# Kernel tuning notes

Measured on AMD Instinct MI355X. Metric: run time of the kernel, lower is better.

Reference implementation:

```python
import jax, jax.numpy as jnp
import numpy as np

N_HEAD, D_MODEL, D_HEAD = 16, 1024, 64
SEQ, BATCH = 2048, 2
EPS = 1e-5


def layer_norm(x, g, b):
    mu = jnp.mean(x, axis=-1, keepdims=True)
    var = jnp.var(x, axis=-1, keepdims=True)
    return (x - mu) * jax.lax.rsqrt(var + EPS) * g + b


def pos_table(n_rows, d_model):
    pos = jnp.arange(n_rows, dtype=jnp.float32)[:, None]
    freqs = jnp.power(10000.0, -jnp.arange(0, d_model, 2, dtype=jnp.float32) / d_model)
    ang = pos * freqs  # [n_rows, d_model//2]
    tab = jnp.zeros((n_rows, d_model), dtype=jnp.float32)
    tab = tab.at[:, 0::2].set(jnp.sin(ang))
    tab = tab.at[:, 1::2].set(jnp.cos(ang))
    return tab


def setup_inputs() -> dict:
    key = jax.random.key(0)
    ks = jax.random.split(key, 7)
    s = 0.02
    return {
        "dec_inp": jax.random.normal(ks[0], (SEQ, BATCH, D_MODEL), jnp.float32),
        "Wq": jax.random.normal(ks[1], (N_HEAD * D_HEAD, D_MODEL), jnp.float32) * s,
        "Wkv": jax.random.normal(ks[2], (2 * N_HEAD * D_HEAD, D_MODEL), jnp.float32) * s,
        "Wo": jax.random.normal(ks[3], (D_MODEL, N_HEAD * D_HEAD), jnp.float32) * s,
        "g1": jnp.ones((D_MODEL,), jnp.float32),
        "b1": jnp.zeros((D_MODEL,), jnp.float32),
        "Wff": jax.random.normal(ks[4], (D_MODEL, N_HEAD * D_HEAD), jnp.float32) * s,
        "g2": jnp.ones((D_MODEL,), jnp.float32),
        "b2": jnp.zeros((D_MODEL,), jnp.float32),
    }


def reference(dec_inp, Wq, Wkv, Wo, g1, b1, Wff, g2, b2):
    S, B, D = dec_inp.shape
    scale = 1.0 / (D_HEAD ** 0.5)
    # projections (post-lnorm path, no mems: c == h)
    q = jnp.einsum('ibd,ed->ibe', dec_inp, Wq).reshape(S, B, N_HEAD, D_HEAD)
    kv = jnp.einsum('ibd,ed->ibe', dec_inp, Wkv)
    k, v = jnp.split(kv, 2, axis=-1)
    k = k.reshape(S, B, N_HEAD, D_HEAD)
    v = v.reshape(S, B, N_HEAD, D_HEAD)
    # attention: scores [i, j, b, n], softmax over j (dim=1)
    scores = jnp.einsum('ibnd,jbnd->ijbn', q, k) * scale
    prob = jax.nn.softmax(scores, axis=1)
    vec = jnp.einsum('ijbn,jbnd->ibnd', prob, v).reshape(S, B, N_HEAD * D_HEAD)
    attn_out = jnp.einsum('ibe,de->ibd', vec, Wo)
    out = layer_norm(dec_inp + attn_out, g1, b1)
    # output += ff(output)
    out = out + jnp.einsum('ibe,de->ibd', out, Wff)
    out = layer_norm(out, g2, b2)
    # output += pos_emb(output)  ==  2*out + pe  (pe indexed by shape[1]==batch)
    pe = pos_table(B, D)  # [B, D], broadcasts over seq
    return out + (out + pe)
```

## Files before the change

kernel.cpp:

```cpp
#include <hip/hip_runtime.h>
#include <hip/hip_bf16.h>
#include <math.h>


typedef __bf16 bf16x8 __attribute__((ext_vector_type(8)));
typedef float f32x4  __attribute__((ext_vector_type(4)));

typedef const __attribute__((address_space(1))) unsigned int as1_uint;
typedef __attribute__((address_space(3))) unsigned int as3_uint;

constexpr int S_SEQ = 2048;
constexpr int DH    = 64;

#define WS_MB (1ull << 20)

__device__ __forceinline__ void gload16(void* lds, const void* g) {
  __builtin_amdgcn_global_load_lds((as1_uint*)g, (as3_uint*)lds, 16, 0, 0);
}

__device__ __forceinline__ float fast_exp2(float x) {
  float r;
  asm volatile("v_exp_f32 %0, %1\n\ts_nop 1" : "=v"(r) : "v"(x));
  return r;
}
__device__ __forceinline__ unsigned cvt_pk_bf16(float lo, float hi) {
  unsigned r;
  asm("v_cvt_pk_bf16_f32 %0, %1, %2" : "=v"(r) : "v"(lo), "v"(hi));
  return r;
}

__device__ __forceinline__ void cvt4(const float* __restrict__ in,
                                     __hip_bfloat16* __restrict__ out, int idx) {
  float4 v = ((const float4*)in)[idx];
  uint2 p;
  p.x = cvt_pk_bf16(v.x, v.y);
  p.y = cvt_pk_bf16(v.z, v.w);
  *(uint2*)(out + (size_t)idx * 4) = p;
}

__global__ __launch_bounds__(256)
void prep_kernel(const float* __restrict__ x, const float* __restrict__ Wq,
                 const float* __restrict__ Wkv, const float* __restrict__ Wo,
                 const float* __restrict__ Wff,
                 __hip_bfloat16* __restrict__ Xb,
                 __hip_bfloat16* __restrict__ Wqkv_b,
                 __hip_bfloat16* __restrict__ Wo_b,
                 __hip_bfloat16* __restrict__ Wff_b,
                 float* __restrict__ pe) {
  const int bid = blockIdx.x, t = threadIdx.x;
  if (bid < 4096) {
    cvt4(x, Xb, bid * 256 + t);
  } else if (bid < 5120) {
    cvt4(Wq, Wqkv_b, (bid - 4096) * 256 + t);
  } else if (bid < 7168) {
    cvt4(Wkv, Wqkv_b + 1024 * 1024, (bid - 5120) * 256 + t);
  } else if (bid < 8192) {
    cvt4(Wo, Wo_b, (bid - 7168) * 256 + t);
  } else if (bid < 9216) {
    cvt4(Wff, Wff_b, (bid - 8192) * 256 + t);
  } else {
#pragma unroll
    for (int rep = 0; rep < 2; ++rep) {
      const int k = rep * 256 + t;
      float freq = expf(-(2.0f * (float)k / 1024.0f) * logf(10000.0f));
      pe[2 * k]            = 0.0f;
      pe[2 * k + 1]        = 1.0f;
      pe[1024 + 2 * k]     = sinf(freq);
      pe[1024 + 2 * k + 1] = cosf(freq);
    }
  }
}

template <int MODE, int BN>
__global__ __launch_bounds__(256)
void gemm_bt(const __hip_bfloat16* __restrict__ A,
             const __hip_bfloat16* __restrict__ Bw,
             float* __restrict__ C,
             __hip_bfloat16* __restrict__ Qb,
             __hip_bfloat16* __restrict__ Kb,
             __hip_bfloat16* __restrict__ VTb,
             int Ndim, int Kdim) {
  constexpr int ASZ = 128 * 64 * 2;
  constexpr int BSZ = BN * 64 * 2;
  constexpr int NI  = BN / 32;
  __shared__ __align__(16) char smem[2 * (ASZ + BSZ)];
  const int t = threadIdx.x, w = t >> 6, l = t & 63;
  const int bm = blockIdx.y * 128, bn = blockIdx.x * BN;
  const int m0 = (w >> 1) * 64, n0 = (w & 1) * (BN / 2);
  const int lrow = l >> 3, lcol = l & 7;
  const int ll = l & 15, lg = l >> 4;

  auto stage = [&](char* buf, int kt) {
#pragma unroll
    for (int r = 0; r < 4; ++r) {
      const int chunk = r * 4 + w;
      const int row = chunk * 8 + lrow;
      gload16(buf + chunk * 1024 + l * 16,
              A + (size_t)(bm + row) * Kdim + kt + lcol * 8);
    }
#pragma unroll
    for (int r = 0; r < BN / 32; ++r) {
      const int chunk = r * 4 + w;
      const int row = chunk * 8 + lrow;
      gload16(buf + ASZ + chunk * 1024 + l * 16,
              Bw + (size_t)(bn + row) * Kdim + kt + lcol * 8);
    }
  };

  f32x4 acc[4][NI] = {};

  stage(smem, 0);
  __syncthreads();
  int cur = 0;
  for (int kt = 0; kt < Kdim; kt += 64) {
    char* bufc = smem + cur * (ASZ + BSZ);
    if (kt + 64 < Kdim) stage(smem + (cur ^ 1) * (ASZ + BSZ), kt + 64);
    const char* sA = bufc;
    const char* sB = bufc + ASZ;
#pragma unroll
    for (int ks = 0; ks < 2; ++ks) {
      bf16x8 a[4], bfr[NI];
#pragma unroll
      for (int mi = 0; mi < 4; ++mi)
        a[mi] = *(const bf16x8*)(sA + (m0 + mi * 16 + ll) * 128 + ks * 64 + lg * 16);
#pragma unroll
      for (int ni = 0; ni < NI; ++ni)
        bfr[ni] = *(const bf16x8*)(sB + (n0 + ni * 16 + ll) * 128 + ks * 64 + lg * 16);
#pragma unroll
      for (int mi = 0; mi < 4; ++mi)
#pragma unroll
        for (int ni = 0; ni < NI; ++ni)
          acc[mi][ni] = __builtin_amdgcn_mfma_f32_16x16x32_bf16(
              a[mi], bfr[ni], acc[mi][ni], 0, 0, 0);
    }
    __syncthreads();
    cur ^= 1;
  }

  if (MODE == 0) {
#pragma unroll
    for (int mi = 0; mi < 4; ++mi)
#pragma unroll
      for (int ni = 0; ni < NI; ++ni)
#pragma unroll
        for (int r = 0; r < 4; ++r) {
          const int gm = bm + m0 + mi * 16 + lg * 4 + r;
          const int gn = bn + n0 + ni * 16 + ll;
          C[(size_t)gm * Ndim + gn] = acc[mi][ni][r];
        }
  } else {
    __hip_bfloat16* img = (__hip_bfloat16*)smem;
    const bool isV = (bn >= 2048);
#pragma unroll
    for (int mi = 0; mi < 4; ++mi)
#pragma unroll
      for (int ni = 0; ni < NI; ++ni)
#pragma unroll
        for (int r = 0; r < 4; ++r) {
          const int gml = m0 + mi * 16 + lg * 4 + r;
          const int gnl = n0 + ni * 16 + ll;
          const int off = isV ? gnl * 136 + ((gml & 1) << 6) + (gml >> 1)
                              : gml * 136 + gnl;
          img[off] = __float2bfloat16(acc[mi][ni][r]);
        }
    __syncthreads();
    const int i0 = bm >> 1;
    const int tile0 = bm >> 6;
#pragma unroll
    for (int j = 0; j < 8; ++j) {
      const int c = j * 256 + t;
      uint4 val;
      __hip_bfloat16* dst;
      if (bn < 1024) {
        const int bb = c >> 10, hl = (c >> 9) & 1;
        const int q = c & 511, il = q >> 3, dh0 = (q & 7) * 8;
        val = *(const uint4*)&img[(il * 2 + bb) * 136 + hl * 64 + dh0];
        dst = Qb + ((size_t)(bb * 16 + (bn >> 6) + hl) * 2048 + i0 + il) * 64 + dh0;
      } else if (bn < 2048) {
        const int run = c >> 6, lane = c & 63;
        const int bb = run >> 4, hl = (run >> 3) & 1, th = (run >> 2) & 1,
                  instr = run & 3;
        const int lg2 = lane >> 4, ll2 = lane & 15;
        const int r32 = (ll2 >> 2) * 8 + (ll2 & 3) + ((instr >> 1) << 2);
        const int il = th * 32 + r32;
        const int dh0 = (instr & 1) * 32 + lg2 * 8;
        val = *(const uint4*)&img[(il * 2 + bb) * 136 + hl * 64 + dh0];
        dst = Kb + (size_t)(bb * 16 + ((bn - 1024) >> 6) + hl) * 131072 +
              (size_t)(tile0 + th) * 2048 + instr * 512 + lane * 8;
      } else {
        const int run = c >> 6, lane = c & 63;
        const int bb = run >> 4, hl = (run >> 3) & 1, th = (run >> 2) & 1,
                  df = run & 3;
        const int lg2 = lane >> 4, ll2 = lane & 15;
        const int il0 = th * 32 + lg2 * 8;
        const int gnl = hl * 64 + df * 16 + ll2;
        val = *(const uint4*)&img[gnl * 136 + bb * 64 + il0];
        dst = VTb + (size_t)(bb * 16 + ((bn - 2048) >> 6) + hl) * 131072 +
              (size_t)(tile0 + th) * 2048 + df * 512 + lane * 8;
      }
      *(uint4*)dst = val;
    }
  }
}


#define MFMA_B16 __builtin_amdgcn_mfma_f32_16x16x32_bf16

#define STAGE(bufp, tb)                                                       \
  {                                                                           \
    gload16((bufp) + woff, Kf + (tb) + wl16);                                 \
    gload16((bufp) + 4096 + woff, Vf + (tb) + wl16);                          \
  }

#define COMPUTE(kk, vv)                                                       \
  {                                                                           \
    const f32x4 z = {0.f, 0.f, 0.f, 0.f};                                     \
    f32x4 s0[2], s1[2];                                                       \
    s0[0] = MFMA_B16(kk[0], qf[0][0], z, 0, 0, 0);                            \
    s0[0] = MFMA_B16(kk[1], qf[0][1], s0[0], 0, 0, 0);                        \
    s1[0] = MFMA_B16(kk[2], qf[0][0], z, 0, 0, 0);                            \
    s1[0] = MFMA_B16(kk[3], qf[0][1], s1[0], 0, 0, 0);                        \
    s0[1] = MFMA_B16(kk[0], qf[1][0], z, 0, 0, 0);                            \
    s0[1] = MFMA_B16(kk[1], qf[1][1], s0[1], 0, 0, 0);                        \
    s1[1] = MFMA_B16(kk[2], qf[1][0], z, 0, 0, 0);                            \
    s1[1] = MFMA_B16(kk[3], qf[1][1], s1[1], 0, 0, 0);                        \
    float plm[2];                                                             \
    _Pragma("unroll")                                                         \
    for (int qi = 0; qi < 2; ++qi) {                                          \
      float a = fmaxf(fmaxf(s0[qi][0], s0[qi][1]),                            \
                      fmaxf(s0[qi][2], s0[qi][3]));                           \
      float c = fmaxf(fmaxf(s1[qi][0], s1[qi][1]),                            \
                      fmaxf(s1[qi][2], s1[qi][3]));                           \
      plm[qi] = fmaxf(a, c) * C1;                                             \
    }                                                                         \
    if (__any((plm[0] > mm[0] + THR2) || (plm[1] > mm[1] + THR2))) {          \
      _Pragma("unroll")                                                       \
      for (int qi = 0; qi < 2; ++qi) {                                        \
        float pm = plm[qi];                                                   \
        pm = fmaxf(pm, __shfl_xor(pm, 16));                                   \
        pm = fmaxf(pm, __shfl_xor(pm, 32));                                   \
        const float nm = fmaxf(mm[qi], pm);                                   \
        const float al = fast_exp2(mm[qi] - nm);                              \
        mm[qi] = nm;                                                          \
        float aR[4];                                                          \
        _Pragma("unroll")                                                     \
        for (int r = 0; r < 4; ++r) aR[r] = __shfl(al, 4 * lg + r);           \
        _Pragma("unroll")                                                     \
        for (int df = 0; df < 4; ++df)                                        \
          _Pragma("unroll")                                                   \
          for (int r = 0; r < 4; ++r) oacc[qi][df][r] *= aR[r];               \
        _Pragma("unroll")                                                     \
        for (int r = 0; r < 4; ++r) oaccS[qi][r] *= aR[r];                    \
      }                                                                       \
    }                                                                         \
    _Pragma("unroll")                                                         \
    for (int qi = 0; qi < 2; ++qi) {                                          \
      float p[8];                                                             \
      _Pragma("unroll")                                                       \
      for (int r = 0; r < 4; ++r) {                                           \
        p[r]     = fast_exp2(fmaf(s0[qi][r], C1, -mm[qi]));                   \
        p[4 + r] = fast_exp2(fmaf(s1[qi][r], C1, -mm[qi]));                   \
      }                                                                       \
      union { unsigned u[4]; bf16x8 v; } pk;                                  \
      pk.u[0] = cvt_pk_bf16(p[0], p[1]);                                      \
      pk.u[1] = cvt_pk_bf16(p[2], p[3]);                                      \
      pk.u[2] = cvt_pk_bf16(p[4], p[5]);                                      \
      pk.u[3] = cvt_pk_bf16(p[6], p[7]);                                      \
      _Pragma("unroll")                                                       \
      for (int df = 0; df < 4; ++df)                                          \
        oacc[qi][df] = MFMA_B16(pk.v, vv[df], oacc[qi][df], 0, 0, 0);         \
      oaccS[qi] = MFMA_B16(pk.v, onesv.v, oaccS[qi], 0, 0, 0);                \
    }                                                                         \
  }

__global__ __launch_bounds__(256)
void attn_kernel(const __hip_bfloat16* __restrict__ Qb,
                 const __hip_bfloat16* __restrict__ Kb,
                 const __hip_bfloat16* __restrict__ VTb,
                 __hip_bfloat16* __restrict__ vec) {
  __shared__ __align__(16) char lds0[8192];
  __shared__ __align__(16) char lds1[8192];
  const int t = threadIdx.x, w = t >> 6, l = t & 63;
  const int bid = blockIdx.x;
  const int slot = bid >> 3;
  const int bh = (bid & 7) * 4 + (slot & 3);
  const int qt = slot >> 2;
  const int b = bh >> 4, h = bh & 15;
  const __hip_bfloat16* Q = Qb + (size_t)bh * S_SEQ * DH;
  const char* Kf = (const char*)Kb + (size_t)bh * 262144;
  const char* Vf = (const char*)VTb + (size_t)bh * 262144;
  const int ll = l & 15, lg = l >> 4;
  const int l16 = l * 16;
  const int woff = w * 1024 + l16;
  const int wl16 = woff;
  constexpr float C1   = 0.125f * 1.44269504088896f;
  constexpr float THR2 = 11.5416f;

  const int qbase = qt * 128 + w * 32;
  bf16x8 qf[2][2];
#pragma unroll
  for (int qi = 0; qi < 2; ++qi) {
    qf[qi][0] = *(const bf16x8*)(Q + (size_t)(qbase + qi * 16 + ll) * 64 + lg * 8);
    qf[qi][1] = *(const bf16x8*)(Q + (size_t)(qbase + qi * 16 + ll) * 64 + 32 + lg * 8);
  }

  union { unsigned u[4]; bf16x8 v; } onesv;
  onesv.u[0] = 0x3F803F80u; onesv.u[1] = 0x3F803F80u;
  onesv.u[2] = 0x3F803F80u; onesv.u[3] = 0x3F803F80u;

  float mm[2] = {-1e30f, -1e30f};
  f32x4 oacc[2][4] = {};
  f32x4 oaccS[2] = {};

  STAGE(lds0, 0);

  for (int tile = 0; tile < 64; ++tile) {
    __syncthreads();
    const char* cur = (tile & 1) ? lds1 : lds0;
    char* nxt       = (tile & 1) ? lds0 : lds1;
    if (tile < 63) STAGE(nxt, (tile + 1) * 4096);
    bf16x8 kk[4], vv[4];
#pragma unroll
    for (int i = 0; i < 4; ++i) {
      kk[i] = *(const bf16x8*)(cur + i * 1024 + l16);
      vv[i] = *(const bf16x8*)(cur + 4096 + i * 1024 + l16);
    }
    COMPUTE(kk, vv);
  }

#pragma unroll
  for (int qi = 0; qi < 2; ++qi) {
    float invR[4];
#pragma unroll
    for (int r = 0; r < 4; ++r) invR[r] = 1.0f / oaccS[qi][r];
#pragma unroll
    for (int df = 0; df < 4; ++df)
#pragma unroll
      for (int r = 0; r < 4; ++r) {
        const int row = qbase + qi * 16 + 4 * lg + r;
        const int e = h * 64 + df * 16 + ll;
        vec[((size_t)row * 2 + b) * 1024 + e] =
            __float2bfloat16(oacc[qi][df][r] * invR[r]);
      }
  }
}

__global__ __launch_bounds__(256)
void add_ln_kernel(const float* __restrict__ X, const float* __restrict__ Yadd,
                   const float* __restrict__ g, const float* __restrict__ bb,
                   float* __restrict__ out_f32,
                   __hip_bfloat16* __restrict__ out_b16) {
  const int row = blockIdx.x, t = threadIdx.x;
  const float4 x4 = *(const float4*)(X + (size_t)row * 1024 + t * 4);
  const float4 a4 = *(const float4*)(Yadd + (size_t)row * 1024 + t * 4);
  float v[4] = {x4.x + a4.x, x4.y + a4.y, x4.z + a4.z, x4.w + a4.w};
  float s = v[0] + v[1] + v[2] + v[3];
  float s2 = v[0] * v[0] + v[1] * v[1] + v[2] * v[2] + v[3] * v[3];
#pragma unroll
  for (int off = 1; off < 64; off <<= 1) {
    s += __shfl_xor(s, off);
    s2 += __shfl_xor(s2, off);
  }
  __shared__ float rs[4], rs2[4];
  if ((t & 63) == 0) { rs[t >> 6] = s; rs2[t >> 6] = s2; }
  __syncthreads();
  const float tot = rs[0] + rs[1] + rs[2] + rs[3];
  const float tot2 = rs2[0] + rs2[1] + rs2[2] + rs2[3];
  const float mu = tot * (1.0f / 1024.0f);
  const float var = tot2 * (1.0f / 1024.0f) - mu * mu;
  const float rstd = rsqrtf(var + 1e-5f);
  const float4 g4 = *(const float4*)(g + t * 4);
  const float4 b4 = *(const float4*)(bb + t * 4);
  float y[4];
  y[0] = (v[0] - mu) * rstd * g4.x + b4.x;
  y[1] = (v[1] - mu) * rstd * g4.y + b4.y;
  y[2] = (v[2] - mu) * rstd * g4.z + b4.z;
  y[3] = (v[3] - mu) * rstd * g4.w + b4.w;
  *(float4*)(out_f32 + (size_t)row * 1024 + t * 4) =
      make_float4(y[0], y[1], y[2], y[3]);
  uint2 pk2;
  pk2.x = cvt_pk_bf16(y[0], y[1]);
  pk2.y = cvt_pk_bf16(y[2], y[3]);
  *(uint2*)(out_b16 + (size_t)row * 1024 + t * 4) = pk2;
}

__global__ __launch_bounds__(256)
void final_kernel(const float* __restrict__ X, const float* __restrict__ Yadd,
                  const float* __restrict__ g, const float* __restrict__ bb,
                  const float* __restrict__ pe, float* __restrict__ out) {
  const int row = blockIdx.x, t = threadIdx.x;
  const float4 x4 = *(const float4*)(X + (size_t)row * 1024 + t * 4);
  const float4 a4 = *(const float4*)(Yadd + (size_t)row * 1024 + t * 4);
  float v[4] = {x4.x + a4.x, x4.y + a4.y, x4.z + a4.z, x4.w + a4.w};
  float s = v[0] + v[1] + v[2] + v[3];
  float s2 = v[0] * v[0] + v[1] * v[1] + v[2] * v[2] + v[3] * v[3];
#pragma unroll
  for (int off = 1; off < 64; off <<= 1) {
    s += __shfl_xor(s, off);
    s2 += __shfl_xor(s2, off);
  }
  __shared__ float rs[4], rs2[4];
  if ((t & 63) == 0) { rs[t >> 6] = s; rs2[t >> 6] = s2; }
  __syncthreads();
  const float tot = rs[0] + rs[1] + rs[2] + rs[3];
  const float tot2 = rs2[0] + rs2[1] + rs2[2] + rs2[3];
  const float mu = tot * (1.0f / 1024.0f);
  const float var = tot2 * (1.0f / 1024.0f) - mu * mu;
  const float rstd = rsqrtf(var + 1e-5f);
  const float4 g4 = *(const float4*)(g + t * 4);
  const float4 b4 = *(const float4*)(bb + t * 4);
  const int bidx = row & 1;
  const float4 p4 = *(const float4*)(pe + bidx * 1024 + t * 4);
  float y[4];
  y[0] = 2.0f * ((v[0] - mu) * rstd * g4.x + b4.x) + p4.x;
  y[1] = 2.0f * ((v[1] - mu) * rstd * g4.y + b4.y) + p4.y;
  y[2] = 2.0f * ((v[2] - mu) * rstd * g4.z + b4.z) + p4.z;
  y[3] = 2.0f * ((v[3] - mu) * rstd * g4.w + b4.w) + p4.w;
  *(float4*)(out + (size_t)row * 1024 + t * 4) = make_float4(y[0], y[1], y[2], y[3]);
}

extern "C" void kernel_launch(void* const* d_in, const int* in_sizes, int n_in,
                              void* d_out, int out_size, void* d_ws,
                              size_t ws_size, hipStream_t stream) {
  const float* x   = (const float*)d_in[0];
  const float* Wq  = (const float*)d_in[1];
  const float* Wkv = (const float*)d_in[2];
  const float* Wo  = (const float*)d_in[3];
  const float* g1  = (const float*)d_in[4];
  const float* b1  = (const float*)d_in[5];
  const float* Wff = (const float*)d_in[6];
  const float* g2  = (const float*)d_in[7];
  const float* b2  = (const float*)d_in[8];

  char* ws = (char*)d_ws;
  __hip_bfloat16* Wqkv_b = (__hip_bfloat16*)(ws + 0);
  __hip_bfloat16* Wo_b   = (__hip_bfloat16*)(ws + 6 * WS_MB);
  __hip_bfloat16* Wff_b  = (__hip_bfloat16*)(ws + 8 * WS_MB);
  __hip_bfloat16* Xb     = (__hip_bfloat16*)(ws + 10 * WS_MB);
  __hip_bfloat16* Qb     = (__hip_bfloat16*)(ws + 18 * WS_MB);
  __hip_bfloat16* Kb     = (__hip_bfloat16*)(ws + 26 * WS_MB);
  __hip_bfloat16* VTb    = (__hip_bfloat16*)(ws + 34 * WS_MB);
  __hip_bfloat16* vecb   = (__hip_bfloat16*)(ws + 42 * WS_MB);
  float* attn            = (float*)(ws + 18 * WS_MB);
  float* out1            = (float*)(ws + 50 * WS_MB);
  __hip_bfloat16* out1b  = (__hip_bfloat16*)(ws + 66 * WS_MB);
  float* ffb             = (float*)(ws + 34 * WS_MB);
  float* pe              = (float*)(ws + 74 * WS_MB);

  prep_kernel<<<9217, 256, 0, stream>>>(x, Wq, Wkv, Wo, Wff, Xb, Wqkv_b,
                                        Wo_b, Wff_b, pe);
  gemm_bt<1, 128><<<dim3(24, 32), 256, 0, stream>>>(Xb, Wqkv_b, nullptr, Qb,
                                                    Kb, VTb, 3072, 1024);
  attn_kernel<<<dim3(512), 256, 0, stream>>>(Qb, Kb, VTb, vecb);
  gemm_bt<0, 64><<<dim3(16, 32), 256, 0, stream>>>(vecb, Wo_b, attn, nullptr,
                                                   nullptr, nullptr, 1024, 1024);
  add_ln_kernel<<<4096, 256, 0, stream>>>(x, attn, g1, b1, out1, out1b);
  gemm_bt<0, 64><<<dim3(16, 32), 256, 0, stream>>>(out1b, Wff_b, ffb, nullptr,
                                                   nullptr, nullptr, 1024, 1024);
  final_kernel<<<4096, 256, 0, stream>>>(out1, ffb, g2, b2, pe, (float*)d_out);
}
```

Measured before the change: 163.1 us.

## Split attention KV range in two with merge kernel, add MFMA priority hints

The attention kernel now splits each query tile's key/value sequence into two halves, launching twice as many blocks. Each block writes a normalized partial output plus its row max and sum, and a new merge kernel combines the two halves with log-sum-exp weights. This raises parallelism from 512 to 1024 blocks to fill more CUs, at the cost of extra partial-output traffic, a second launch and bf16 rounding of the partials. s_setprio hints are also placed around the MFMA groups to favour matrix issue across waves.

```diff
diff --git a/kernel.cpp b/kernel.cpp
--- a/kernel.cpp
+++ b/kernel.cpp
@@ -216,6 +216,7 @@
   {                                                                           \
     const f32x4 z = {0.f, 0.f, 0.f, 0.f};                                     \
     f32x4 s0[2], s1[2];                                                       \
+    __builtin_amdgcn_s_setprio(1);                                            \
     s0[0] = MFMA_B16(kk[0], qf[0][0], z, 0, 0, 0);                            \
     s0[0] = MFMA_B16(kk[1], qf[0][1], s0[0], 0, 0, 0);                        \
     s1[0] = MFMA_B16(kk[2], qf[0][0], z, 0, 0, 0);                            \
@@ -224,6 +225,7 @@
     s0[1] = MFMA_B16(kk[1], qf[1][1], s0[1], 0, 0, 0);                        \
     s1[1] = MFMA_B16(kk[2], qf[1][0], z, 0, 0, 0);                            \
     s1[1] = MFMA_B16(kk[3], qf[1][1], s1[1], 0, 0, 0);                        \
+    __builtin_amdgcn_s_setprio(0);                                            \
     float plm[2];                                                             \
     _Pragma("unroll")                                                         \
     for (int qi = 0; qi < 2; ++qi) {                                          \
@@ -266,10 +268,12 @@
       pk.u[1] = cvt_pk_bf16(p[2], p[3]);                                      \
       pk.u[2] = cvt_pk_bf16(p[4], p[5]);                                      \
       pk.u[3] = cvt_pk_bf16(p[6], p[7]);                                      \
+      __builtin_amdgcn_s_setprio(1);                                          \
       _Pragma("unroll")                                                       \
       for (int df = 0; df < 4; ++df)                                          \
         oacc[qi][df] = MFMA_B16(pk.v, vv[df], oacc[qi][df], 0, 0, 0);         \
       oaccS[qi] = MFMA_B16(pk.v, onesv.v, oaccS[qi], 0, 0, 0);                \
+      __builtin_amdgcn_s_setprio(0);                                          \
     }                                                                         \
   }
 
@@ -277,14 +281,16 @@
 void attn_kernel(const __hip_bfloat16* __restrict__ Qb,
                  const __hip_bfloat16* __restrict__ Kb,
                  const __hip_bfloat16* __restrict__ VTb,
-                 __hip_bfloat16* __restrict__ vec) {
+                 __hip_bfloat16* __restrict__ po,
+                 float2* __restrict__ ml) {
   __shared__ __align__(16) char lds0[8192];
   __shared__ __align__(16) char lds1[8192];
   const int t = threadIdx.x, w = t >> 6, l = t & 63;
   const int bid = blockIdx.x;
   const int slot = bid >> 3;
   const int bh = (bid & 7) * 4 + (slot & 3);
-  const int qt = slot >> 2;
+  const int kvhalf = (slot >> 2) & 1;
+  const int qt = slot >> 3;
   const int b = bh >> 4, h = bh & 15;
   const __hip_bfloat16* Q = Qb + (size_t)bh * S_SEQ * DH;
   const char* Kf = (const char*)Kb + (size_t)bh * 262144;
@@ -293,6 +299,9 @@
   const int l16 = l * 16;
   const int woff = w * 1024 + l16;
   const int wl16 = woff;
+  const int tb0 = kvhalf * 131072;
+  const size_t poHalf = (size_t)kvhalf * 4194304;
+  const int mlHalf = kvhalf * 65536;
   constexpr float C1   = 0.125f * 1.44269504088896f;
   constexpr float THR2 = 11.5416f;
 
@@ -312,13 +321,13 @@
   f32x4 oacc[2][4] = {};
   f32x4 oaccS[2] = {};
 
-  STAGE(lds0, 0);
-
-  for (int tile = 0; tile < 64; ++tile) {
+  STAGE(lds0, tb0);
+
+  for (int tile = 0; tile < 32; ++tile) {
     __syncthreads();
     const char* cur = (tile & 1) ? lds1 : lds0;
     char* nxt       = (tile & 1) ? lds0 : lds1;
-    if (tile < 63) STAGE(nxt, (tile + 1) * 4096);
+    if (tile < 31) STAGE(nxt, tb0 + (tile + 1) * 4096);
     bf16x8 kk[4], vv[4];
 #pragma unroll
     for (int i = 0; i < 4; ++i) {
@@ -330,19 +339,63 @@
 
 #pragma unroll
   for (int qi = 0; qi < 2; ++qi) {
-    float invR[4];
-#pragma unroll
-    for (int r = 0; r < 4; ++r) invR[r] = 1.0f / oaccS[qi][r];
+    float mC[4], lC[4], invR[4];
+#pragma unroll
+    for (int r = 0; r < 4; ++r) {
+      mC[r] = __shfl(mm[qi], 4 * lg + r);
+      lC[r] = oaccS[qi][r];
+      invR[r] = 1.0f / lC[r];
+    }
 #pragma unroll
     for (int df = 0; df < 4; ++df)
 #pragma unroll
       for (int r = 0; r < 4; ++r) {
-        const int row = qbase + qi * 16 + 4 * lg + r;
+        const int q = qbase + qi * 16 + 4 * lg + r;
         const int e = h * 64 + df * 16 + ll;
-        vec[((size_t)row * 2 + b) * 1024 + e] =
+        po[poHalf + ((size_t)q * 2 + b) * 1024 + e] =
             __float2bfloat16(oacc[qi][df][r] * invR[r]);
       }
-  }
+    if (ll == 0) {
+#pragma unroll
+      for (int r = 0; r < 4; ++r) {
+        const int q = qbase + qi * 16 + 4 * lg + r;
+        ml[mlHalf + bh * 2048 + q] = make_float2(mC[r], lC[r]);
+      }
+    }
+  }
+}
+
+__global__ __launch_bounds__(256)
+void merge_kernel(const __hip_bfloat16* __restrict__ po,
+                  const float2* __restrict__ ml,
+                  __hip_bfloat16* __restrict__ vec) {
+  const int row = blockIdx.x, t = threadIdx.x;
+  const int e0 = t * 4, h = e0 >> 6;
+  const int b = row & 1, i = row >> 1;
+  const int idx = (b * 16 + h) * 2048 + i;
+  const float2 ml0 = ml[idx];
+  const float2 ml1 = ml[65536 + idx];
+  const float M = fmaxf(ml0.x, ml1.x);
+  float a0 = ml0.y * fast_exp2(ml0.x - M);
+  float a1 = ml1.y * fast_exp2(ml1.x - M);
+  const float inv = 1.0f / (a0 + a1);
+  a0 *= inv; a1 *= inv;
+  const size_t off = (size_t)row * 1024 + e0;
+  const uint2 u0 = *(const uint2*)(po + off);
+  const uint2 u1 = *(const uint2*)(po + 4194304 + off);
+  float out[4];
+#pragma unroll
+  for (int j = 0; j < 4; ++j) {
+    const unsigned s0 = ((j < 2 ? u0.x : u0.y) >> (16 * (j & 1))) & 0xFFFFu;
+    const unsigned s1 = ((j < 2 ? u1.x : u1.y) >> (16 * (j & 1))) & 0xFFFFu;
+    union { unsigned u; float f; } c0, c1;
+    c0.u = s0 << 16; c1.u = s1 << 16;
+    out[j] = a0 * c0.f + a1 * c1.f;
+  }
+  uint2 pk2;
+  pk2.x = cvt_pk_bf16(out[0], out[1]);
+  pk2.y = cvt_pk_bf16(out[2], out[3]);
+  *(uint2*)(vec + off) = pk2;
 }
 
 __global__ __launch_bounds__(256)
@@ -442,6 +495,8 @@
   __hip_bfloat16* VTb    = (__hip_bfloat16*)(ws + 34 * WS_MB);
   __hip_bfloat16* vecb   = (__hip_bfloat16*)(ws + 42 * WS_MB);
   float* attn            = (float*)(ws + 18 * WS_MB);
+  __hip_bfloat16* po     = (__hip_bfloat16*)(ws + 50 * WS_MB);
+  float2* ml             = (float2*)(ws + 67 * WS_MB);
   float* out1            = (float*)(ws + 50 * WS_MB);
   __hip_bfloat16* out1b  = (__hip_bfloat16*)(ws + 66 * WS_MB);
   float* ffb             = (float*)(ws + 34 * WS_MB);
@@ -451,7 +506,8 @@
                                         Wo_b, Wff_b, pe);
   gemm_bt<1, 128><<<dim3(24, 32), 256, 0, stream>>>(Xb, Wqkv_b, nullptr, Qb,
                                                     Kb, VTb, 3072, 1024);
-  attn_kernel<<<dim3(512), 256, 0, stream>>>(Qb, Kb, VTb, vecb);
+  attn_kernel<<<dim3(1024), 256, 0, stream>>>(Qb, Kb, VTb, po, ml);
+  merge_kernel<<<dim3(4096), 256, 0, stream>>>(po, ml, vecb);
   gemm_bt<0, 64><<<dim3(16, 32), 256, 0, stream>>>(vecb, Wo_b, attn, nullptr,
                                                    nullptr, nullptr, 1024, 1024);
   add_ln_kernel<<<4096, 256, 0, stream>>>(x, attn, g1, b1, out1, out1b);
```

New measurement: 173.3 us. +6.3%, slower.

## Deepen attention K/V prefetch to 4-stage ring with vmcnt waits and MFMA priority

Applied to the files above, without the earlier changes.

Replaces the double-buffered K/V LDS staging with a four-slot ring that keeps three tiles in flight, using explicit s_waitcnt vmcnt counts and raw barriers instead of __syncthreads. This is meant to hide global-load latency better. It also raises wave priority around the MFMA sequences via s_setprio so matrix work issues ahead of other waves. LDS use grows from 16KB to 32KB per block, which may reduce occupancy, and correctness depends on the vmcnt accounting matching the two loads per stage.

```diff
diff --git a/kernel.cpp b/kernel.cpp
--- a/kernel.cpp
+++ b/kernel.cpp
@@ -216,6 +216,7 @@
   {                                                                           \
     const f32x4 z = {0.f, 0.f, 0.f, 0.f};                                     \
     f32x4 s0[2], s1[2];                                                       \
+    __builtin_amdgcn_s_setprio(1);                                            \
     s0[0] = MFMA_B16(kk[0], qf[0][0], z, 0, 0, 0);                            \
     s0[0] = MFMA_B16(kk[1], qf[0][1], s0[0], 0, 0, 0);                        \
     s1[0] = MFMA_B16(kk[2], qf[0][0], z, 0, 0, 0);                            \
@@ -224,6 +225,7 @@
     s0[1] = MFMA_B16(kk[1], qf[1][1], s0[1], 0, 0, 0);                        \
     s1[1] = MFMA_B16(kk[2], qf[1][0], z, 0, 0, 0);                            \
     s1[1] = MFMA_B16(kk[3], qf[1][1], s1[1], 0, 0, 0);                        \
+    __builtin_amdgcn_s_setprio(0);                                            \
     float plm[2];                                                             \
     _Pragma("unroll")                                                         \
     for (int qi = 0; qi < 2; ++qi) {                                          \
@@ -266,11 +268,29 @@
       pk.u[1] = cvt_pk_bf16(p[2], p[3]);                                      \
       pk.u[2] = cvt_pk_bf16(p[4], p[5]);                                      \
       pk.u[3] = cvt_pk_bf16(p[6], p[7]);                                      \
+      __builtin_amdgcn_s_setprio(1);                                          \
       _Pragma("unroll")                                                       \
       for (int df = 0; df < 4; ++df)                                          \
         oacc[qi][df] = MFMA_B16(pk.v, vv[df], oacc[qi][df], 0, 0, 0);         \
       oaccS[qi] = MFMA_B16(pk.v, onesv.v, oaccS[qi], 0, 0, 0);                \
+      __builtin_amdgcn_s_setprio(0);                                          \
     }                                                                         \
+  }
+
+#define PHASE(tile_, vmN_, doStage_)                                          \
+  {                                                                           \
+    asm volatile("s_waitcnt vmcnt(" #vmN_ ")" ::: "memory");                  \
+    __builtin_amdgcn_s_barrier();                                             \
+    if (doStage_) STAGE(lds + (((tile_) + 3) & 3) * 8192,                     \
+                        ((tile_) + 3) * 4096);                                \
+    const char* cur = lds + ((tile_) & 3) * 8192;                             \
+    bf16x8 kk[4], vv[4];                                                      \
+    _Pragma("unroll")                                                         \
+    for (int i = 0; i < 4; ++i) {                                             \
+      kk[i] = *(const bf16x8*)(cur + i * 1024 + l16);                         \
+      vv[i] = *(const bf16x8*)(cur + 4096 + i * 1024 + l16);                  \
+    }                                                                         \
+    COMPUTE(kk, vv);                                                          \
   }
 
 __global__ __launch_bounds__(256)
@@ -278,8 +298,7 @@
                  const __hip_bfloat16* __restrict__ Kb,
                  const __hip_bfloat16* __restrict__ VTb,
                  __hip_bfloat16* __restrict__ vec) {
-  __shared__ __align__(16) char lds0[8192];
-  __shared__ __align__(16) char lds1[8192];
+  __shared__ __align__(16) char lds[4 * 8192];
   const int t = threadIdx.x, w = t >> 6, l = t & 63;
   const int bid = blockIdx.x;
   const int slot = bid >> 3;
@@ -312,21 +331,14 @@
   f32x4 oacc[2][4] = {};
   f32x4 oaccS[2] = {};
 
-  STAGE(lds0, 0);
-
-  for (int tile = 0; tile < 64; ++tile) {
-    __syncthreads();
-    const char* cur = (tile & 1) ? lds1 : lds0;
-    char* nxt       = (tile & 1) ? lds0 : lds1;
-    if (tile < 63) STAGE(nxt, (tile + 1) * 4096);
-    bf16x8 kk[4], vv[4];
-#pragma unroll
-    for (int i = 0; i < 4; ++i) {
-      kk[i] = *(const bf16x8*)(cur + i * 1024 + l16);
-      vv[i] = *(const bf16x8*)(cur + 4096 + i * 1024 + l16);
-    }
-    COMPUTE(kk, vv);
-  }
+  STAGE(lds, 0);
+  STAGE(lds + 8192, 4096);
+  STAGE(lds + 16384, 8192);
+
+  for (int tile = 0; tile < 61; ++tile) PHASE(tile, 4, true);
+  PHASE(61, 4, false);
+  PHASE(62, 2, false);
+  PHASE(63, 0, false);
 
 #pragma unroll
   for (int qi = 0; qi < 2; ++qi) {
```

Result: no change. 164.2 us (+0.7%).
